# Performance work log

Hardware: AMD Instinct MI355X
Metric: run time of the kernel (lower is better)

## Reference

```python
import jax, jax.numpy as jnp
import numpy as np

# CIM / quantization constants hardcoded in the source module
INPUT_BIT = 8
WEIGHT_BIT = 4
OUTPUT_BIT = 8
DAC_BIT = 2
ADC_BIT = 8
ADC_GAIN_1_SCALE = 1.0 / 63.0
GAIN_MIN, GAIN_MAX = 1.0, 255.0
N_SLICES = INPUT_BIT // DAC_BIT  # 4 bit-serial input slices of 2 bits each


def ste_round(v):
    # straight-through round: forward = round(v), backward = identity
    return v + jax.lax.stop_gradient(jnp.round(v) - v)


def conv2d(x, w):
    # NCHW conv, stride 1, padding k//2 (SAME for odd k)
    return jax.lax.conv_general_dilated(
        x, w, window_strides=(1, 1), padding='SAME',
        dimension_numbers=('NCHW', 'OIHW', 'NCHW'))


def setup_inputs() -> dict:
    key = jax.random.key(0)
    kx, kw, kb = jax.random.split(key, 3)
    B, Cin, H, W = 16, 4, 512, 512
    Cout, K = 8, 3
    x = jax.random.uniform(kx, (B, Cin, H, W), dtype=jnp.float32)  # non-negative activations
    weight = jax.random.normal(kw, (Cout, Cin, K, K), dtype=jnp.float32) * 0.05
    bias = jax.random.normal(kb, (Cout,), dtype=jnp.float32) * 0.01
    s_in = jnp.float32(1.0 / 255.0)   # LSQ input scale (8-bit unsigned)
    s_w = jnp.float32(0.02)           # LSQ weight scale (4-bit signed)
    s_out = jnp.float32(0.05)         # LSQ output scale (8-bit signed)
    return {"x": x, "weight": weight, "bias": bias,
            "s_in": s_in, "s_w": s_w, "s_out": s_out}


def reference(x, weight, bias, s_in, s_w, s_out):
    in_max = 2.0 ** INPUT_BIT - 1.0          # 255
    w_lim = 2.0 ** (WEIGHT_BIT - 1) - 1.0    # 7
    adc_max = 2.0 ** (ADC_BIT - 1) - 1.0     # 127
    o_lim = 2.0 ** (OUTPUT_BIT - 1) - 1.0    # 127
    base = float(2 ** DAC_BIT)               # 4 levels per DAC slice

    # LSQ quantization of input (unsigned) and weight (signed), STE rounding
    xq = jnp.clip(ste_round(x / s_in), 0.0, in_max)        # integer-valued floats
    wq = jnp.clip(ste_round(weight / s_w), -w_lim, w_lim)

    # ideal integer conv (gradient path)
    ideal = conv2d(xq, wq)

    # bit-serial DAC/ADC CIM path (forward only; noise_scale=0 so no noise)
    xi = jax.lax.stop_gradient(xq)
    wi = jax.lax.stop_gradient(wq)
    psums = []
    for s in range(N_SLICES):
        sl = jnp.mod(jnp.floor(xi / (base ** s)), base)    # 2-bit slice in [0,3]
        psums.append(conv2d(sl, wi))
    # ADC gain adjustment ('gain' mode): integer gain in [1,255], LSB = 1/(gain*gain_1_scale)
    p_absmax = jnp.maximum(
        jnp.max(jnp.stack([jnp.max(jnp.abs(p)) for p in psums])), 1e-6)
    gain = jnp.clip(jnp.round(adc_max / (p_absmax * ADC_GAIN_1_SCALE)),
                    GAIN_MIN, GAIN_MAX)
    step = 1.0 / (gain * ADC_GAIN_1_SCALE)
    acc = jnp.zeros_like(ideal)
    for s, p in enumerate(psums):
        adc_out = jnp.clip(jnp.round(p / step), -adc_max, adc_max) * step
        acc = acc + adc_out * (base ** s)

    # straight-through: forward uses analog path, backward uses ideal conv
    psum = ideal + jax.lax.stop_gradient(acc - ideal)

    out = psum * (s_in * s_w) + bias[None, :, None, None]
    # LSQ output quantization (8-bit signed)
    out = jnp.clip(ste_round(out / s_out), -o_lim, o_lim) * s_out
    return out
```

## Files before the change

kernel.cpp:

```cpp
#include <hip/hip_runtime.h>
#include <stdint.h>

#define B_   16
#define CIN  4
#define COUT 8
#define H_   512
#define W_   512
#define HP   (H_ + 2)
#define WP   (W_ + 2)
#define PMAX 756
#define TBL  (2 * PMAX + 1)
#define RPB  8
#define GY   (H_ / RPB)
#define NBLK (2 * GY * B_)
#define NQ   (B_ * HP)

__device__ __forceinline__ int dot4(uint32_t a, int b, int c) {
#if __has_builtin(__builtin_amdgcn_sdot4)
    return __builtin_amdgcn_sdot4((int)a, b, c, false);
#else
    int r = c;
#pragma unroll
    for (int i = 0; i < 4; ++i) {
        int av = (int)((a >> (8 * i)) & 0xFFu);
        int bv = ((int)(((uint32_t)b) << (24 - 8 * i))) >> 24;
        r += av * bv;
    }
    return r;
#endif
}

__device__ __forceinline__ int dot8(uint32_t a, int b, int c) {
#if __has_builtin(__builtin_amdgcn_sdot8)
    return __builtin_amdgcn_sdot8((int)a, b, c, false);
#else
    int r = c;
#pragma unroll
    for (int i = 0; i < 8; ++i) {
        int av = (int)((a >> (4 * i)) & 0xFu);
        int bv = ((int)(((uint32_t)b) << (28 - 4 * i))) >> 28;
        r += av * bv;
    }
    return r;
#endif
}

__device__ __forceinline__ float rfl_f(float v) {
    return __int_as_float(__builtin_amdgcn_readfirstlane(__float_as_int(v)));
}

__device__ __forceinline__ int wquant(const float* w, float s_w,
                                      int co, int ci, int tap) {
    const int kh = tap / 3, kw = tap % 3;
    float wv = w[((co * CIN + ci) * 3 + kh) * 3 + kw];
    float q  = rintf(__fdiv_rn(wv, s_w));
    q = fminf(fmaxf(q, -7.0f), 7.0f);
    return (int)q;
}

__global__ __launch_bounds__(128) void quant_pack_kernel(
        const float* __restrict__ x, const float* __restrict__ weight,
        const float* __restrict__ s_in_p, const float* __restrict__ s_w_p,
        uint32_t* __restrict__ xq, uint32_t* __restrict__ wq8) {
    const int raw = blockIdx.x;
    const int lin = (raw & 7) * (NQ / 8) + (raw >> 3);
    const int b = lin / HP, hp = lin % HP;
    const int t = threadIdx.x;
    if (raw == 0) {
        const float s_w = *s_w_p;
        if (t < 32) {
            const int co = t >> 2, p = t & 3;
            const int tA = (p == 0) ? 0 : (p == 1) ? 3 : (p == 2) ? 6 : 2;
            const int tB = (p == 0) ? 1 : (p == 1) ? 4 : (p == 2) ? 7 : 5;
            uint32_t v = 0;
#pragma unroll
            for (int ci = 0; ci < CIN; ++ci) {
                v |= ((uint32_t)(wquant(weight, s_w, co, ci, tA) & 0xF)) << (8 * ci);
                v |= ((uint32_t)(wquant(weight, s_w, co, ci, tB) & 0xF)) << (8 * ci + 4);
            }
            wq8[t] = v;
        } else if (t < 40) {
            const int co = t - 32;
            uint32_t v = 0;
#pragma unroll
            for (int ci = 0; ci < CIN; ++ci)
                v |= ((uint32_t)(wquant(weight, s_w, co, ci, 8) & 0xFF)) << (8 * ci);
            wq8[32 + co] = v;
        }
    }
    uint32_t* dst = xq + ((size_t)b * HP + hp) * WP;
    if (hp == 0 || hp == HP - 1) {
        for (int i = t; i < WP; i += 128) dst[i] = 0;
        return;
    }
    const float s_in = *s_in_p;
    const int h = hp - 1;
    const size_t plane = (size_t)H_ * W_;
    const float* xr = x + ((size_t)b * CIN) * plane + (size_t)h * W_ + 4 * t;
    float4 v0 = *(const float4*)(xr);
    float4 v1 = *(const float4*)(xr + plane);
    float4 v2 = *(const float4*)(xr + 2 * plane);
    float4 v3 = *(const float4*)(xr + 3 * plane);
    uint32_t o0 = 0, o1 = 0, o2 = 0, o3 = 0;
#define QP(f, ci, oj)                                                  \
    { float q = rintf(__fdiv_rn((f), s_in));                           \
      q = fminf(fmaxf(q, 0.0f), 255.0f);                               \
      oj |= ((uint32_t)(int)q) << (8 * (ci)); }
    QP(v0.x, 0, o0) QP(v0.y, 0, o1) QP(v0.z, 0, o2) QP(v0.w, 0, o3)
    QP(v1.x, 1, o0) QP(v1.y, 1, o1) QP(v1.z, 1, o2) QP(v1.w, 1, o3)
    QP(v2.x, 2, o0) QP(v2.y, 2, o1) QP(v2.z, 2, o2) QP(v2.w, 2, o3)
    QP(v3.x, 3, o0) QP(v3.y, 3, o1) QP(v3.z, 3, o2) QP(v3.w, 3, o3)
#undef QP
    uint32_t* d = dst + 1 + 4 * t;
    d[0] = o0; d[1] = o1; d[2] = o2; d[3] = o3;
    if (t == 0) dst[0] = 0;
    if (t == 127) dst[WP - 1] = 0;
}

#define LOADW()                                                              \
    int w8s[32], w4s[8];                                                     \
    {                                                                        \
        const int4* q4 = (const int4*)wq8;                                   \
        _Pragma("unroll")                                                    \
        for (int i = 0; i < 8; ++i) {                                        \
            int4 w4i = q4[i];                                                \
            w8s[4 * i + 0] = __builtin_amdgcn_readfirstlane(w4i.x);          \
            w8s[4 * i + 1] = __builtin_amdgcn_readfirstlane(w4i.y);          \
            w8s[4 * i + 2] = __builtin_amdgcn_readfirstlane(w4i.z);          \
            w8s[4 * i + 3] = __builtin_amdgcn_readfirstlane(w4i.w);          \
        }                                                                    \
        int4 a0 = q4[8], a1 = q4[9];                                         \
        w4s[0] = __builtin_amdgcn_readfirstlane(a0.x);                       \
        w4s[1] = __builtin_amdgcn_readfirstlane(a0.y);                       \
        w4s[2] = __builtin_amdgcn_readfirstlane(a0.z);                       \
        w4s[3] = __builtin_amdgcn_readfirstlane(a0.w);                       \
        w4s[4] = __builtin_amdgcn_readfirstlane(a1.x);                       \
        w4s[5] = __builtin_amdgcn_readfirstlane(a1.y);                       \
        w4s[6] = __builtin_amdgcn_readfirstlane(a1.z);                       \
        w4s[7] = __builtin_amdgcn_readfirstlane(a1.w);                       \
    }

#define SWZ()                                                                \
    const int raw = blockIdx.x;                                              \
    const int lin = (raw & 7) * (NBLK / 8) + (raw >> 3);                     \
    const int bx = lin & 1;                                                  \
    const int hy = (lin >> 1) & (GY - 1);                                    \
    const int b  = lin >> 7;                                                 \
    const int w0 = bx * 256 + threadIdx.x;                                   \
    const int h0 = hy * RPB;

#define EXTS(CA, SG, v0, v1, v2)                                             \
    do {                                                                     \
        uint32_t lo_ = ((v0) & 0x0F0F0F0Fu) | (((v1) << 4) & 0xF0F0F0F0u);   \
        uint32_t hi_ = (((v0) >> 4) & 0x0F0F0F0Fu) | ((v1) & 0xF0F0F0F0u);   \
        CA[0] = lo_ & 0x33333333u;                                           \
        CA[1] = (lo_ >> 2) & 0x33333333u;                                    \
        CA[2] = hi_ & 0x33333333u;                                           \
        CA[3] = (hi_ >> 2) & 0x33333333u;                                    \
        SG[0] = (v2)&0x03030303u;                                            \
        SG[1] = ((v2) >> 2) & 0x03030303u;                                   \
        SG[2] = ((v2) >> 4) & 0x03030303u;                                   \
        SG[3] = ((v2) >> 6) & 0x03030303u;                                   \
    } while (0)

#define RING_INIT()                                                          \
    uint32_t cA0[4], cA1[4], cA2[4], cA3[4];                                 \
    uint32_t sg0[4], sg1[4], sg2[4], sg3[4];                                 \
    {                                                                        \
        uint32_t r0 = base[0], r1 = base[1], r2 = base[2];                   \
        EXTS(cA0, sg0, r0, r1, r2);                                          \
        r0 = base[WP]; r1 = base[WP + 1]; r2 = base[WP + 2];                 \
        EXTS(cA1, sg1, r0, r1, r2);                                          \
    }                                                                        \
    uint32_t n0 = base[2 * WP], n1 = base[2 * WP + 1], n2 = base[2 * WP + 2];

#define PREF(S)                                                              \
    if ((S) < RPB - 1) {                                                     \
        const uint32_t* nr_ = base + (size_t)((S) + 3) * WP;                 \
        n0 = nr_[0]; n1 = nr_[1]; n2 = nr_[2];                               \
    }

#define DOTS(CAa, SGa, CAb, SGb, CAc, SGc, K, INIT, OUTV)                    \
    {                                                                        \
        int a_ = dot4(SGc[K], w4s[co], INIT);                                \
        a_ = dot8(CAa[K], w8s[co * 4 + 0], a_);                              \
        a_ = dot8(CAb[K], w8s[co * 4 + 1], a_);                              \
        a_ = dot8(CAc[K], w8s[co * 4 + 2], a_);                              \
        a_ = dot8(K == 0 ? pc0 : K == 1 ? pc1 : K == 2 ? pc2 : pc3,          \
                  w8s[co * 4 + 3], a_);                                      \
        OUTV = a_;                                                           \
    }

#define STEP1(S, CAa, SGa, CAb, SGb, CAc, SGc)                               \
    do {                                                                     \
        EXTS(CAc, SGc, n0, n1, n2);                                          \
        PREF(S);                                                             \
        const uint32_t pc0 = SGa[0] | (SGb[0] << 4);                         \
        const uint32_t pc1 = SGa[1] | (SGb[1] << 4);                         \
        const uint32_t pc2 = SGa[2] | (SGb[2] << 4);                         \
        const uint32_t pc3 = SGa[3] | (SGb[3] << 4);                         \
        _Pragma("unroll")                                                    \
        for (int co = 0; co < COUT; ++co) {                                  \
            int a0, a1, a2, a3;                                              \
            DOTS(CAa, SGa, CAb, SGb, CAc, SGc, 0, 0, a0);                    \
            DOTS(CAa, SGa, CAb, SGb, CAc, SGc, 1, 0, a1);                    \
            DOTS(CAa, SGa, CAb, SGb, CAc, SGc, 2, 0, a2);                    \
            DOTS(CAa, SGa, CAb, SGb, CAc, SGc, 3, 0, a3);                    \
            rMax0 = max(rMax0, a0); rMin0 = min(rMin0, a0);                  \
            rMax1 = max(rMax1, a1); rMin1 = min(rMin1, a1);                  \
            rMax2 = max(rMax2, a2); rMin2 = min(rMin2, a2);                  \
            rMax3 = max(rMax3, a3); rMin3 = min(rMin3, a3);                  \
        }                                                                    \
    } while (0)

__global__ __launch_bounds__(256, 8) void conv_absmax(
        const uint32_t* __restrict__ xq, const uint32_t* __restrict__ wq8,
        int* __restrict__ blkmax) {
    __shared__ int red[4];
    LOADW();
    SWZ();
    const uint32_t* base = xq + ((size_t)b * HP + h0) * WP + w0;
    RING_INIT();
    int rMax0 = 0, rMax1 = 0, rMax2 = 0, rMax3 = 0;
    int rMin0 = 0, rMin1 = 0, rMin2 = 0, rMin3 = 0;
    STEP1(0, cA0, sg0, cA1, sg1, cA2, sg2);
    STEP1(1, cA1, sg1, cA2, sg2, cA3, sg3);
    STEP1(2, cA2, sg2, cA3, sg3, cA0, sg0);
    STEP1(3, cA3, sg3, cA0, sg0, cA1, sg1);
    STEP1(4, cA0, sg0, cA1, sg1, cA2, sg2);
    STEP1(5, cA1, sg1, cA2, sg2, cA3, sg3);
    STEP1(6, cA2, sg2, cA3, sg3, cA0, sg0);
    STEP1(7, cA3, sg3, cA0, sg0, cA1, sg1);
    int m = max(max(max(rMax0, -rMin0), max(rMax1, -rMin1)),
                max(max(rMax2, -rMin2), max(rMax3, -rMin3)));
#pragma unroll
    for (int off = 1; off < 64; off <<= 1)
        m = max(m, __shfl_xor(m, off));
    if ((threadIdx.x & 63) == 0) red[threadIdx.x >> 6] = m;
    __syncthreads();
    if (threadIdx.x == 0)
        blkmax[raw] = max(max(red[0], red[1]), max(red[2], red[3]));
}

__global__ __launch_bounds__(256) void reduce_absmax(
        const int* __restrict__ blkmax, int* __restrict__ absmax) {
    __shared__ int red[4];
    const int t = threadIdx.x;
    int m = 0;
#pragma unroll
    for (int i = 0; i < NBLK / 256; ++i) m = max(m, blkmax[t + 256 * i]);
#pragma unroll
    for (int off = 1; off < 64; off <<= 1)
        m = max(m, __shfl_xor(m, off));
    if ((t & 63) == 0) red[t >> 6] = m;
    __syncthreads();
    if (t == 0)
        *absmax = max(max(red[0], red[1]), max(red[2], red[3]));
}

#define STEP2(S, CAa, SGa, CAb, SGb, CAc, SGc)                               \
    do {                                                                     \
        EXTS(CAc, SGc, n0, n1, n2);                                          \
        PREF(S);                                                             \
        const uint32_t pc0 = SGa[0] | (SGb[0] << 4);                         \
        const uint32_t pc1 = SGa[1] | (SGb[1] << 4);                         \
        const uint32_t pc2 = SGa[2] | (SGb[2] << 4);                         \
        const uint32_t pc3 = SGa[3] | (SGb[3] << 4);                         \
        int ax[COUT][4];                                                     \
        _Pragma("unroll")                                                    \
        for (int co = 0; co < COUT; ++co) {                                  \
            DOTS(CAa, SGa, CAb, SGb, CAc, SGc, 0, PMAX, ax[co][0]);          \
            DOTS(CAa, SGa, CAb, SGb, CAc, SGc, 1, PMAX, ax[co][1]);          \
            DOTS(CAa, SGa, CAb, SGb, CAc, SGc, 2, PMAX, ax[co][2]);          \
            DOTS(CAa, SGa, CAb, SGb, CAc, SGc, 3, PMAX, ax[co][3]);          \
        }                                                                    \
        float tv[COUT][4];                                                   \
        _Pragma("unroll")                                                    \
        for (int co = 0; co < COUT; ++co) {                                  \
            tv[co][0] = T0[ax[co][0]];                                       \
            tv[co][1] = T4[ax[co][1]];                                       \
            tv[co][2] = T0[ax[co][2]];                                       \
            tv[co][3] = T4[ax[co][3]];                                       \
        }                                                                    \
        float* orow = out + ((size_t)b * COUT * H_ + (size_t)(h0 + (S))) * W_ + w0; \
        _Pragma("unroll")                                                    \
        for (int co = 0; co < COUT; ++co) {                                  \
            float of = __fadd_rn(tv[co][0], tv[co][1]);                      \
            of = __fadd_rn(of, __fmul_rn(tv[co][2], 16.0f));                 \
            of = __fadd_rn(of, __fmul_rn(tv[co][3], 16.0f));                 \
            float o_ = __fadd_rn(__fmul_rn(of, scale), br[co]);              \
            float q0 = __fmul_rn(o_, y1);        \
            float rr = fmaf(-s_out, q0, o_);                                 \
            float qd = fmaf(rr, y1, q0);                                     \
            float q_ = rintf(qd);                                            \
            q_ = fminf(fmaxf(q_, -127.0f), 127.0f);                          \
            orow[(size_t)co * plane] = __fmul_rn(q_, s_out);                 \
        }                                                                    \
    } while (0)

__global__ __launch_bounds__(256) void conv_out(
        const uint32_t* __restrict__ xq, const uint32_t* __restrict__ wq8,
        const float* __restrict__ bias, const float* __restrict__ sp_in,
        const float* __restrict__ sp_w, const float* __restrict__ sp_out,
        const int* __restrict__ absmax, float* __restrict__ out) {
    __shared__ float T0[TBL];
    __shared__ float T4[TBL];
    LOADW();
    const float pabs = fmaxf((float)(*absmax), 1e-6f);
    const float c63  = 1.0f / 63.0f;
    float g = rintf(__fdiv_rn(127.0f, __fmul_rn(pabs, c63)));
    g = fminf(fmaxf(g, 1.0f), 255.0f);
    const float step = __fdiv_rn(1.0f, __fmul_rn(g, c63));
    for (int i = threadIdx.x; i < TBL; i += 256) {
        float p = (float)(i - PMAX);
        float r = rintf(__fdiv_rn(p, step));
        r = fminf(fmaxf(r, -127.0f), 127.0f);
        float v = __fmul_rn(r, step);
        T0[i] = v;
        T4[i] = 4.0f * v;
    }
    const float scale = __fmul_rn(rfl_f(*sp_in), rfl_f(*sp_w));
    const float s_out = rfl_f(*sp_out);
    float y0 = __builtin_amdgcn_rcpf(s_out);
    float e  = fmaf(-s_out, y0, 1.0f);
    const float y1 = fmaf(y0, e, y0);
    float br[COUT];
#pragma unroll
    for (int co = 0; co < COUT; ++co) br[co] = rfl_f(bias[co]);
    __syncthreads();

    SWZ();
    const uint32_t* base = xq + ((size_t)b * HP + h0) * WP + w0;
    const size_t plane = (size_t)H_ * W_;
    RING_INIT();
    STEP2(0, cA0, sg0, cA1, sg1, cA2, sg2);
    STEP2(1, cA1, sg1, cA2, sg2, cA3, sg3);
    STEP2(2, cA2, sg2, cA3, sg3, cA0, sg0);
    STEP2(3, cA3, sg3, cA0, sg0, cA1, sg1);
    STEP2(4, cA0, sg0, cA1, sg1, cA2, sg2);
    STEP2(5, cA1, sg1, cA2, sg2, cA3, sg3);
    STEP2(6, cA2, sg2, cA3, sg3, cA0, sg0);
    STEP2(7, cA3, sg3, cA0, sg0, cA1, sg1);
}

extern "C" void kernel_launch(void* const* d_in, const int* in_sizes, int n_in,
                              void* d_out, int out_size, void* d_ws, size_t ws_size,
                              hipStream_t stream) {
    const float* x      = (const float*)d_in[0];
    const float* weight = (const float*)d_in[1];
    const float* bias   = (const float*)d_in[2];
    const float* s_in   = (const float*)d_in[3];
    const float* s_w    = (const float*)d_in[4];
    const float* s_out  = (const float*)d_in[5];
    float* out = (float*)d_out;

    int*      absmax = (int*)d_ws;
    uint32_t* wq8    = (uint32_t*)((char*)d_ws + 256);
    int*      blkmax = (int*)((char*)d_ws + 1024);
    uint32_t* xq     = (uint32_t*)((char*)d_ws + 16384);

    quant_pack_kernel<<<dim3(NQ), dim3(128), 0, stream>>>(
        x, weight, s_in, s_w, xq, wq8);

    conv_absmax<<<dim3(NBLK), dim3(256), 0, stream>>>(xq, wq8, blkmax);

    reduce_absmax<<<dim3(1), dim3(256), 0, stream>>>(blkmax, absmax);

    conv_out<<<dim3(NBLK), dim3(256), 0, stream>>>(
        xq, wq8, bias, s_in, s_w, s_out, absmax, out);
}
```

Measured before the change: 92.97 us.

## Fuse input quantization into absmax conv pass and replace reduction with atomicMax

After: 104.7 us. 1.13x slower.

```diff
diff --git a/kernel.cpp b/kernel.cpp
--- a/kernel.cpp
+++ b/kernel.cpp
@@ -13,7 +13,6 @@
 #define RPB  8
 #define GY   (H_ / RPB)
 #define NBLK (2 * GY * B_)
-#define NQ   (B_ * HP)
 
 __device__ __forceinline__ int dot4(uint32_t a, int b, int c) {
 #if __has_builtin(__builtin_amdgcn_sdot4)
@@ -47,6 +46,16 @@
 
 __device__ __forceinline__ float rfl_f(float v) {
     return __int_as_float(__builtin_amdgcn_readfirstlane(__float_as_int(v)));
+}
+__device__ __forceinline__ float recip1(float d) {
+    float y0 = __builtin_amdgcn_rcpf(d);
+    float e  = fmaf(-d, y0, 1.0f);
+    return fmaf(y0, e, y0);
+}
+__device__ __forceinline__ float mdiv(float n, float d, float y) {
+    float q0 = __fmul_rn(n, y);
+    float rr = fmaf(-d, q0, n);
+    return fmaf(rr, y, q0);
 }
 
 __device__ __forceinline__ int wquant(const float* w, float s_w,
@@ -58,87 +67,35 @@
     return (int)q;
 }
 
-__global__ __launch_bounds__(128) void quant_pack_kernel(
-        const float* __restrict__ x, const float* __restrict__ weight,
-        const float* __restrict__ s_in_p, const float* __restrict__ s_w_p,
-        uint32_t* __restrict__ xq, uint32_t* __restrict__ wq8) {
-    const int raw = blockIdx.x;
-    const int lin = (raw & 7) * (NQ / 8) + (raw >> 3);
-    const int b = lin / HP, hp = lin % HP;
-    const int t = threadIdx.x;
-    if (raw == 0) {
-        const float s_w = *s_w_p;
-        if (t < 32) {
-            const int co = t >> 2, p = t & 3;
-            const int tA = (p == 0) ? 0 : (p == 1) ? 3 : (p == 2) ? 6 : 2;
-            const int tB = (p == 0) ? 1 : (p == 1) ? 4 : (p == 2) ? 7 : 5;
-            uint32_t v = 0;
-#pragma unroll
-            for (int ci = 0; ci < CIN; ++ci) {
-                v |= ((uint32_t)(wquant(weight, s_w, co, ci, tA) & 0xF)) << (8 * ci);
-                v |= ((uint32_t)(wquant(weight, s_w, co, ci, tB) & 0xF)) << (8 * ci + 4);
-            }
-            wq8[t] = v;
-        } else if (t < 40) {
-            const int co = t - 32;
-            uint32_t v = 0;
-#pragma unroll
-            for (int ci = 0; ci < CIN; ++ci)
-                v |= ((uint32_t)(wquant(weight, s_w, co, ci, 8) & 0xFF)) << (8 * ci);
-            wq8[32 + co] = v;
-        }
-    }
-    uint32_t* dst = xq + ((size_t)b * HP + hp) * WP;
-    if (hp == 0 || hp == HP - 1) {
-        for (int i = t; i < WP; i += 128) dst[i] = 0;
-        return;
-    }
-    const float s_in = *s_in_p;
-    const int h = hp - 1;
-    const size_t plane = (size_t)H_ * W_;
-    const float* xr = x + ((size_t)b * CIN) * plane + (size_t)h * W_ + 4 * t;
-    float4 v0 = *(const float4*)(xr);
-    float4 v1 = *(const float4*)(xr + plane);
-    float4 v2 = *(const float4*)(xr + 2 * plane);
-    float4 v3 = *(const float4*)(xr + 3 * plane);
-    uint32_t o0 = 0, o1 = 0, o2 = 0, o3 = 0;
-#define QP(f, ci, oj)                                                  \
-    { float q = rintf(__fdiv_rn((f), s_in));                           \
-      q = fminf(fmaxf(q, 0.0f), 255.0f);                               \
-      oj |= ((uint32_t)(int)q) << (8 * (ci)); }
-    QP(v0.x, 0, o0) QP(v0.y, 0, o1) QP(v0.z, 0, o2) QP(v0.w, 0, o3)
-    QP(v1.x, 1, o0) QP(v1.y, 1, o1) QP(v1.z, 1, o2) QP(v1.w, 1, o3)
-    QP(v2.x, 2, o0) QP(v2.y, 2, o1) QP(v2.z, 2, o2) QP(v2.w, 2, o3)
-    QP(v3.x, 3, o0) QP(v3.y, 3, o1) QP(v3.z, 3, o2) QP(v3.w, 3, o3)
-#undef QP
-    uint32_t* d = dst + 1 + 4 * t;
-    d[0] = o0; d[1] = o1; d[2] = o2; d[3] = o3;
-    if (t == 0) dst[0] = 0;
-    if (t == 127) dst[WP - 1] = 0;
-}
-
-#define LOADW()                                                              \
+#define WPREP(wlds_, weight_, swv_)                                          \
+    if (t < 40) {                                                            \
+        uint32_t v = 0;                                                      \
+        if (t < 32) {                                                        \
+            const int co = t >> 2, p = t & 3;                                \
+            const int tA = (p == 0) ? 0 : (p == 1) ? 3 : (p == 2) ? 6 : 2;   \
+            const int tB = (p == 0) ? 1 : (p == 1) ? 4 : (p == 2) ? 7 : 5;   \
+            _Pragma("unroll")                                                \
+            for (int ci = 0; ci < CIN; ++ci) {                               \
+                v |= ((uint32_t)(wquant(weight_, swv_, co, ci, tA) & 0xF)) << (8 * ci);      \
+                v |= ((uint32_t)(wquant(weight_, swv_, co, ci, tB) & 0xF)) << (8 * ci + 4);  \
+            }                                                                \
+        } else {                                                             \
+            const int co = t - 32;                                           \
+            _Pragma("unroll")                                                \
+            for (int ci = 0; ci < CIN; ++ci)                                 \
+                v |= ((uint32_t)(wquant(weight_, swv_, co, ci, 8) & 0xFF)) << (8 * ci);      \
+        }                                                                    \
+        wlds_[t] = v;                                                        \
+    }
+
+#define LOADW_LDS(wlds_)                                                     \
     int w8s[32], w4s[8];                                                     \
-    {                                                                        \
-        const int4* q4 = (const int4*)wq8;                                   \
-        _Pragma("unroll")                                                    \
-        for (int i = 0; i < 8; ++i) {                                        \
-            int4 w4i = q4[i];                                                \
-            w8s[4 * i + 0] = __builtin_amdgcn_readfirstlane(w4i.x);          \
-            w8s[4 * i + 1] = __builtin_amdgcn_readfirstlane(w4i.y);          \
-            w8s[4 * i + 2] = __builtin_amdgcn_readfirstlane(w4i.z);          \
-            w8s[4 * i + 3] = __builtin_amdgcn_readfirstlane(w4i.w);          \
-        }                                                                    \
-        int4 a0 = q4[8], a1 = q4[9];                                         \
-        w4s[0] = __builtin_amdgcn_readfirstlane(a0.x);                       \
-        w4s[1] = __builtin_amdgcn_readfirstlane(a0.y);                       \
-        w4s[2] = __builtin_amdgcn_readfirstlane(a0.z);                       \
-        w4s[3] = __builtin_amdgcn_readfirstlane(a0.w);                       \
-        w4s[4] = __builtin_amdgcn_readfirstlane(a1.x);                       \
-        w4s[5] = __builtin_amdgcn_readfirstlane(a1.y);                       \
-        w4s[6] = __builtin_amdgcn_readfirstlane(a1.z);                       \
-        w4s[7] = __builtin_amdgcn_readfirstlane(a1.w);                       \
-    }
+    _Pragma("unroll")                                                        \
+    for (int i = 0; i < 32; ++i)                                             \
+        w8s[i] = __builtin_amdgcn_readfirstlane((int)wlds_[i]);              \
+    _Pragma("unroll")                                                        \
+    for (int i = 0; i < 8; ++i)                                              \
+        w4s[i] = __builtin_amdgcn_readfirstlane((int)wlds_[32 + i]);
 
 #define SWZ()                                                                \
     const int raw = blockIdx.x;                                              \
@@ -163,23 +120,6 @@
         SG[3] = ((v2) >> 6) & 0x03030303u;                                   \
     } while (0)
 
-#define RING_INIT()                                                          \
-    uint32_t cA0[4], cA1[4], cA2[4], cA3[4];                                 \
-    uint32_t sg0[4], sg1[4], sg2[4], sg3[4];                                 \
-    {                                                                        \
-        uint32_t r0 = base[0], r1 = base[1], r2 = base[2];                   \
-        EXTS(cA0, sg0, r0, r1, r2);                                          \
-        r0 = base[WP]; r1 = base[WP + 1]; r2 = base[WP + 2];                 \
-        EXTS(cA1, sg1, r0, r1, r2);                                          \
-    }                                                                        \
-    uint32_t n0 = base[2 * WP], n1 = base[2 * WP + 1], n2 = base[2 * WP + 2];
-
-#define PREF(S)                                                              \
-    if ((S) < RPB - 1) {                                                     \
-        const uint32_t* nr_ = base + (size_t)((S) + 3) * WP;                 \
-        n0 = nr_[0]; n1 = nr_[1]; n2 = nr_[2];                               \
-    }
-
 #define DOTS(CAa, SGa, CAb, SGb, CAc, SGc, K, INIT, OUTV)                    \
     {                                                                        \
         int a_ = dot4(SGc[K], w4s[co], INIT);                                \
@@ -191,10 +131,93 @@
         OUTV = a_;                                                           \
     }
 
-#define STEP1(S, CAa, SGa, CAb, SGb, CAc, SGc)                               \
-    do {                                                                     \
-        EXTS(CAc, SGc, n0, n1, n2);                                          \
-        PREF(S);                                                             \
+__device__ __forceinline__ uint32_t qone(float fv, float s_in, float yin) {
+    float q = rintf(mdiv(fv, s_in, yin));
+    q = fminf(fmaxf(q, 0.0f), 255.0f);
+    return (uint32_t)(int)q;
+}
+
+__global__ __launch_bounds__(256, 6) void conv_absmax_fused(
+        const float* __restrict__ x, const float* __restrict__ weight,
+        const float* __restrict__ s_in_p, const float* __restrict__ s_w_p,
+        uint32_t* __restrict__ xq, int* __restrict__ absmax) {
+    __shared__ uint32_t wlds[40];
+    __shared__ int red[4];
+    const int t = threadIdx.x;
+    {
+        const float s_w = *s_w_p;
+        WPREP(wlds, weight, s_w);
+    }
+    SWZ();
+    const float s_in = *s_in_p;
+    const float yin  = recip1(s_in);
+    __syncthreads();
+    LOADW_LDS(wlds);
+
+    const int c = w0;
+    const size_t plane = (size_t)H_ * W_;
+    const float* xb = x + (size_t)b * CIN * plane;
+    uint32_t* xqb = xq + (size_t)b * HP * WP;
+
+    if (hy == 0)
+        for (int i = t; i < WP; i += 256) xqb[i] = 0;
+    if (hy == GY - 1)
+        for (int i = t; i < WP; i += 256) xqb[(size_t)(HP - 1) * WP + i] = 0;
+    if (t == 0) {
+        const int col = (bx == 0) ? 0 : (WP - 1);
+#pragma unroll
+        for (int r = 0; r < RPB; ++r)
+            xqb[(size_t)(h0 + 1 + r) * WP + col] = 0;
+    }
+
+    float f0, f1, f2, f3;
+#define LOADR(d)                                                             \
+    do {                                                                     \
+        if ((unsigned)(d) < (unsigned)H_) {                                  \
+            const float* p_ = xb + (size_t)(d)*W_ + c;                       \
+            f0 = p_[0]; f1 = p_[plane]; f2 = p_[2 * plane]; f3 = p_[3 * plane]; \
+        } else { f0 = f1 = f2 = f3 = 0.0f; }                                 \
+    } while (0)
+
+#define QDIR(d, cc) __extension__({                                         \
+    uint32_t v_ = 0;                                                         \
+    if ((unsigned)(d) < (unsigned)H_ && (unsigned)(cc) < (unsigned)W_) {     \
+        const float* p_ = xb + (size_t)(d)*W_ + (cc);                        \
+        v_ = qone(p_[0], s_in, yin) | (qone(p_[plane], s_in, yin) << 8) |    \
+             (qone(p_[2 * plane], s_in, yin) << 16) |                        \
+             (qone(p_[3 * plane], s_in, yin) << 24);                         \
+    }                                                                        \
+    v_; })
+
+#define QSTEP(d, CA, SG)                                                     \
+    do {                                                                     \
+        uint32_t M_ = qone(f0, s_in, yin) | (qone(f1, s_in, yin) << 8) |     \
+                      (qone(f2, s_in, yin) << 16) | (qone(f3, s_in, yin) << 24); \
+        uint32_t L_ = __shfl_up(M_, 1);                                      \
+        uint32_t R_ = __shfl_down(M_, 1);                                    \
+        if ((t & 63) == 0)  L_ = QDIR((d), c - 1);                           \
+        if ((t & 63) == 63) R_ = QDIR((d), c + 1);                           \
+        if ((d) >= h0 && (d) <= h0 + RPB - 1)                                \
+            xqb[(size_t)((d) + 1) * WP + (c + 1)] = M_;                      \
+        EXTS(CA, SG, L_, M_, R_);                                            \
+    } while (0)
+
+    uint32_t cA0[4], cA1[4], cA2[4], cA3[4];
+    uint32_t sg0[4], sg1[4], sg2[4], sg3[4];
+
+    LOADR(h0 - 1);
+    QSTEP(h0 - 1, cA0, sg0);
+    LOADR(h0);
+    QSTEP(h0, cA1, sg1);
+    LOADR(h0 + 1);
+
+    int rMax0 = 0, rMax1 = 0, rMax2 = 0, rMax3 = 0;
+    int rMin0 = 0, rMin1 = 0, rMin2 = 0, rMin3 = 0;
+
+#define STEP1F(S, CAa, SGa, CAb, SGb, CAc, SGc)                              \
+    do {                                                                     \
+        QSTEP(h0 + (S) + 1, CAc, SGc);                                       \
+        if ((S) < RPB - 1) LOADR(h0 + (S) + 2);                              \
         const uint32_t pc0 = SGa[0] | (SGb[0] << 4);                         \
         const uint32_t pc1 = SGa[1] | (SGb[1] << 4);                         \
         const uint32_t pc2 = SGa[2] | (SGb[2] << 4);                         \
@@ -213,50 +236,42 @@
         }                                                                    \
     } while (0)
 
-__global__ __launch_bounds__(256, 8) void conv_absmax(
-        const uint32_t* __restrict__ xq, const uint32_t* __restrict__ wq8,
-        int* __restrict__ blkmax) {
-    __shared__ int red[4];
-    LOADW();
-    SWZ();
-    const uint32_t* base = xq + ((size_t)b * HP + h0) * WP + w0;
-    RING_INIT();
-    int rMax0 = 0, rMax1 = 0, rMax2 = 0, rMax3 = 0;
-    int rMin0 = 0, rMin1 = 0, rMin2 = 0, rMin3 = 0;
-    STEP1(0, cA0, sg0, cA1, sg1, cA2, sg2);
-    STEP1(1, cA1, sg1, cA2, sg2, cA3, sg3);
-    STEP1(2, cA2, sg2, cA3, sg3, cA0, sg0);
-    STEP1(3, cA3, sg3, cA0, sg0, cA1, sg1);
-    STEP1(4, cA0, sg0, cA1, sg1, cA2, sg2);
-    STEP1(5, cA1, sg1, cA2, sg2, cA3, sg3);
-    STEP1(6, cA2, sg2, cA3, sg3, cA0, sg0);
-    STEP1(7, cA3, sg3, cA0, sg0, cA1, sg1);
+    STEP1F(0, cA0, sg0, cA1, sg1, cA2, sg2);
+    STEP1F(1, cA1, sg1, cA2, sg2, cA3, sg3);
+    STEP1F(2, cA2, sg2, cA3, sg3, cA0, sg0);
+    STEP1F(3, cA3, sg3, cA0, sg0, cA1, sg1);
+    STEP1F(4, cA0, sg0, cA1, sg1, cA2, sg2);
+    STEP1F(5, cA1, sg1, cA2, sg2, cA3, sg3);
+    STEP1F(6, cA2, sg2, cA3, sg3, cA0, sg0);
+    STEP1F(7, cA3, sg3, cA0, sg0, cA1, sg1);
+
     int m = max(max(max(rMax0, -rMin0), max(rMax1, -rMin1)),
                 max(max(rMax2, -rMin2), max(rMax3, -rMin3)));
-#pragma unroll
-    for (int off = 1; off < 64; off <<= 1)
-        m = max(m, __shfl_xor(m, off));
-    if ((threadIdx.x & 63) == 0) red[threadIdx.x >> 6] = m;
-    __syncthreads();
-    if (threadIdx.x == 0)
-        blkmax[raw] = max(max(red[0], red[1]), max(red[2], red[3]));
-}
-
-__global__ __launch_bounds__(256) void reduce_absmax(
-        const int* __restrict__ blkmax, int* __restrict__ absmax) {
-    __shared__ int red[4];
-    const int t = threadIdx.x;
-    int m = 0;
-#pragma unroll
-    for (int i = 0; i < NBLK / 256; ++i) m = max(m, blkmax[t + 256 * i]);
 #pragma unroll
     for (int off = 1; off < 64; off <<= 1)
         m = max(m, __shfl_xor(m, off));
     if ((t & 63) == 0) red[t >> 6] = m;
     __syncthreads();
     if (t == 0)
-        *absmax = max(max(red[0], red[1]), max(red[2], red[3]));
-}
+        atomicMax(absmax, max(max(red[0], red[1]), max(red[2], red[3])));
+}
+
+#define RING_INIT()                                                          \
+    uint32_t cA0[4], cA1[4], cA2[4], cA3[4];                                 \
+    uint32_t sg0[4], sg1[4], sg2[4], sg3[4];                                 \
+    {                                                                        \
+        uint32_t r0 = base[0], r1 = base[1], r2 = base[2];                   \
+        EXTS(cA0, sg0, r0, r1, r2);                                          \
+        r0 = base[WP]; r1 = base[WP + 1]; r2 = base[WP + 2];                 \
+        EXTS(cA1, sg1, r0, r1, r2);                                          \
+    }                                                                        \
+    uint32_t n0 = base[2 * WP], n1 = base[2 * WP + 1], n2 = base[2 * WP + 2];
+
+#define PREF(S)                                                              \
+    if ((S) < RPB - 1) {                                                     \
+        const uint32_t* nr_ = base + (size_t)((S) + 3) * WP;                 \
+        n0 = nr_[0]; n1 = nr_[1]; n2 = nr_[2];                               \
+    }
 
 #define STEP2(S, CAa, SGa, CAb, SGb, CAc, SGc)                               \
     do {                                                                     \
@@ -289,7 +304,7 @@
             of = __fadd_rn(of, __fmul_rn(tv[co][2], 16.0f));                 \
             of = __fadd_rn(of, __fmul_rn(tv[co][3], 16.0f));                 \
             float o_ = __fadd_rn(__fmul_rn(of, scale), br[co]);              \
-            float q0 = __fmul_rn(o_, y1);        \
+            float q0 = __fmul_rn(o_, y1);                                    \
             float rr = fmaf(-s_out, q0, o_);                                 \
             float qd = fmaf(rr, y1, q0);                                     \
             float q_ = rintf(qd);                                            \
@@ -299,19 +314,24 @@
     } while (0)
 
 __global__ __launch_bounds__(256) void conv_out(
-        const uint32_t* __restrict__ xq, const uint32_t* __restrict__ wq8,
+        const uint32_t* __restrict__ xq, const float* __restrict__ weight,
         const float* __restrict__ bias, const float* __restrict__ sp_in,
         const float* __restrict__ sp_w, const float* __restrict__ sp_out,
         const int* __restrict__ absmax, float* __restrict__ out) {
     __shared__ float T0[TBL];
     __shared__ float T4[TBL];
-    LOADW();
+    __shared__ uint32_t wlds[40];
+    const int t = threadIdx.x;
+    {
+        const float s_w = *sp_w;
+        WPREP(wlds, weight, s_w);
+    }
     const float pabs = fmaxf((float)(*absmax), 1e-6f);
     const float c63  = 1.0f / 63.0f;
     float g = rintf(__fdiv_rn(127.0f, __fmul_rn(pabs, c63)));
     g = fminf(fmaxf(g, 1.0f), 255.0f);
     const float step = __fdiv_rn(1.0f, __fmul_rn(g, c63));
-    for (int i = threadIdx.x; i < TBL; i += 256) {
+    for (int i = t; i < TBL; i += 256) {
         float p = (float)(i - PMAX);
         float r = rintf(__fdiv_rn(p, step));
         r = fminf(fmaxf(r, -127.0f), 127.0f);
@@ -321,13 +341,12 @@
     }
     const float scale = __fmul_rn(rfl_f(*sp_in), rfl_f(*sp_w));
     const float s_out = rfl_f(*sp_out);
-    float y0 = __builtin_amdgcn_rcpf(s_out);
-    float e  = fmaf(-s_out, y0, 1.0f);
-    const float y1 = fmaf(y0, e, y0);
+    const float y1    = recip1(s_out);
     float br[COUT];
 #pragma unroll
     for (int co = 0; co < COUT; ++co) br[co] = rfl_f(bias[co]);
     __syncthreads();
+    LOADW_LDS(wlds);
 
     SWZ();
     const uint32_t* base = xq + ((size_t)b * HP + h0) * WP + w0;
@@ -355,17 +374,13 @@
     float* out = (float*)d_out;
 
     int*      absmax = (int*)d_ws;
-    uint32_t* wq8    = (uint32_t*)((char*)d_ws + 256);
-    int*      blkmax = (int*)((char*)d_ws + 1024);
-    uint32_t* xq     = (uint32_t*)((char*)d_ws + 16384);
-
-    quant_pack_kernel<<<dim3(NQ), dim3(128), 0, stream>>>(
-        x, weight, s_in, s_w, xq, wq8);
-
-    conv_absmax<<<dim3(NBLK), dim3(256), 0, stream>>>(xq, wq8, blkmax);
-
-    reduce_absmax<<<dim3(1), dim3(256), 0, stream>>>(blkmax, absmax);
+    uint32_t* xq     = (uint32_t*)((char*)d_ws + 1024);
+
+    hipMemsetAsync(absmax, 0, sizeof(int), stream);
+
+    conv_absmax_fused<<<dim3(NBLK), dim3(256), 0, stream>>>(
+        x, weight, s_in, s_w, xq, absmax);
 
     conv_out<<<dim3(NBLK), dim3(256), 0, stream>>>(
-        xq, wq8, bias, s_in, s_w, s_out, absmax, out);
-}
+        xq, weight, bias, s_in, s_w, s_out, absmax, out);
+}
```
